# Optimization experiments

Measured on AMD Instinct MI355X. Metric: run time of the kernel, lower is better.

The kernel has to match this reference:

```python
import jax, jax.numpy as jnp
import numpy as np

TEMPERATURE = 0.2

def setup_inputs() -> dict:
    key = jax.random.key(0)
    k1, k2 = jax.random.split(key)
    B, D = 4096, 128
    emb_i = jax.random.normal(k1, (B, D), dtype=jnp.float32)
    emb_j = jax.random.normal(k2, (B, D), dtype=jnp.float32)
    return {"emb_i": emb_i, "emb_j": emb_j}

def reference(emb_i, emb_j):
    # L2-normalize each embedding row, concat -> z: [2B, D]
    z_i = emb_i / jnp.linalg.norm(emb_i, axis=1, keepdims=True)
    z_j = emb_j / jnp.linalg.norm(emb_j, axis=1, keepdims=True)
    z = jnp.concatenate([z_i, z_j], axis=0)          # [2B, D]
    N2 = z.shape[0]
    N = N2 // 2
    # cosine similarity of normalized vectors == dot product
    sim = z @ z.T                                    # [2B, 2B]
    logits = sim / TEMPERATURE
    # denominator excludes only the diagonal (k != i)
    diag_mask = jnp.eye(N2, dtype=bool)
    masked = jnp.where(diag_mask, -jnp.inf, logits)
    lse = jax.nn.logsumexp(masked, axis=1)           # [2B]
    # positive pair for row i is i+N (mod 2N)
    pos_idx = jnp.concatenate([jnp.arange(N) + N, jnp.arange(N)])
    pos_logits = jnp.take_along_axis(logits, pos_idx[:, None], axis=1)[:, 0]
    # loss = (1/2N) * sum_i -log( exp(pos_i) / sum_{k!=i} exp(logits[i,k]) )
    loss = jnp.mean(lse - pos_logits)
    return loss
```

## Files before the change

kernel.cpp:

```cpp
#include <hip/hip_runtime.h>
#include <hip/hip_bf16.h>

typedef __attribute__((ext_vector_type(8))) short bf16x8;
typedef __attribute__((ext_vector_type(4))) float f32x4;

#define EXP_SCALE 7.213475204444817f

__device__ __forceinline__ float fast_exp2(float x) {
#if __has_builtin(__builtin_amdgcn_exp2f)
  return __builtin_amdgcn_exp2f(x);
#else
  return exp2f(x);
#endif
}

__device__ __forceinline__ unsigned short f32_to_bf16(float f) {
  unsigned int u = __float_as_uint(f);
  unsigned int r = (u + 0x7FFFu + ((u >> 16) & 1u)) >> 16;
  return (unsigned short)r;
}


__global__ __launch_bounds__(256) void k_normalize(
    const float* __restrict__ emb_i, const float* __restrict__ emb_j,
    unsigned short* __restrict__ z, float* __restrict__ out)
{
  if (blockIdx.x == 0 && threadIdx.x == 0) out[0] = 0.0f;
  const int t = threadIdx.x;
  const int c = t >> 4;
  const int sub = t & 15;
  const int row = (blockIdx.x << 4) + c;
  const float* src = (row < 4096) ? (emb_i + row * 128) : (emb_j + (row - 4096) * 128);
  float4 v0 = reinterpret_cast<const float4*>(src)[sub * 2];
  float4 v1 = reinterpret_cast<const float4*>(src)[sub * 2 + 1];
  float ss = v0.x*v0.x + v0.y*v0.y + v0.z*v0.z + v0.w*v0.w
           + v1.x*v1.x + v1.y*v1.y + v1.z*v1.z + v1.w*v1.w;
  #pragma unroll
  for (int m = 1; m < 16; m <<= 1) ss += __shfl_xor(ss, m, 64);
  float rinv = 1.0f / sqrtf(ss);
  unsigned short st[8];
  st[0] = f32_to_bf16(v0.x * rinv); st[1] = f32_to_bf16(v0.y * rinv);
  st[2] = f32_to_bf16(v0.z * rinv); st[3] = f32_to_bf16(v0.w * rinv);
  st[4] = f32_to_bf16(v1.x * rinv); st[5] = f32_to_bf16(v1.y * rinv);
  st[6] = f32_to_bf16(v1.z * rinv); st[7] = f32_to_bf16(v1.w * rinv);
  unsigned short* dst = z + blockIdx.x * 2048 + (sub >> 2) * 512 +
                        (((sub & 3) << 4) + c) * 8;
  *reinterpret_cast<bf16x8*>(dst) = *reinterpret_cast<bf16x8*>(st);
}

__global__ __launch_bounds__(256, 3) void k_simlse(
    const unsigned short* __restrict__ z,
    float* __restrict__ rpart,
    float* __restrict__ cpart,
    float* __restrict__ rowpos)
{
  const int w = threadIdx.x >> 6;
  const int lane = threadIdx.x & 63;
  const int q = lane >> 4;
  const int c = lane & 15;

  int ch = 0;
  while ((int)blockIdx.x >= 4 * (ch + 1) * (ch + 2)) ++ch;
  const int rb = blockIdx.x - 4 * ch * (ch + 1);
  const int R0 = rb << 6;
  const bool upper = (rb < (ch << 3));

  bf16x8 a[4][4];
  {
    const unsigned short* ap = z + (R0 >> 4) * 2048 + (lane << 3);
    #pragma unroll
    for (int rg = 0; rg < 4; ++rg)
      #pragma unroll
      for (int kk = 0; kk < 4; ++kk)
        a[rg][kk] = *reinterpret_cast<const bf16x8*>(ap + rg * 2048 + kk * 512);
  }

  float acc[4][4];
  #pragma unroll
  for (int rg = 0; rg < 4; ++rg)
    #pragma unroll
    for (int e = 0; e < 4; ++e) acc[rg][e] = 0.0f;
  float pacc[4] = {0.f, 0.f, 0.f, 0.f};
  float colp[8];
  #pragma unroll
  for (int i = 0; i < 8; ++i) colp[i] = 0.0f;

  __shared__ float lsum[4][64];
  __shared__ float lpos[4][16];

  const int ct0 = (ch << 5) + w;
  const unsigned short* bwave = z + ct0 * 2048 + (lane << 3);

  const int pos0t = ((R0 + 4096) & 8191) >> 4;
  const int ipb = ((pos0t >> 5) == ch) ? ((pos0t & 31) >> 2) : -99;

  bf16x8 b0[4], b1[4];
  auto ldb = [&](bf16x8 (&dst)[4], int idx) {
    const unsigned short* p = bwave + idx * 8192;
    dst[0] = *reinterpret_cast<const bf16x8*>(p);
    dst[1] = *reinterpret_cast<const bf16x8*>(p + 512);
    dst[2] = *reinterpret_cast<const bf16x8*>(p + 1024);
    dst[3] = *reinterpret_cast<const bf16x8*>(p + 1536);
  };

  auto process = [&](const bf16x8 (&bb)[4], int i) {
    f32x4 cc[4];
    #pragma unroll
    for (int rr = 0; rr < 4; ++rr) cc[rr] = f32x4{0.f, 0.f, 0.f, 0.f};
    #pragma unroll
    for (int kk = 0; kk < 4; ++kk)
      #pragma unroll
      for (int rr = 0; rr < 4; ++rr)
        cc[rr] = __builtin_amdgcn_mfma_f32_16x16x32_bf16(
            a[rr][kk], bb[kk], cc[rr], 0, 0, 0);
    float cp0 = 0.0f, cp1 = 0.0f;
    #pragma unroll
    for (int rr = 0; rr < 4; ++rr)
      #pragma unroll
      for (int e = 0; e < 4; ++e) {
        float tv = fast_exp2(__builtin_fmaf(cc[rr][e], EXP_SCALE, -EXP_SCALE));
        acc[rr][e] += tv;
        if (upper) { if (rr & 1) cp1 += tv; else cp0 += tv; }
      }
    if (upper) colp[i] = cp0 + cp1;
    if (i == ipb) {
      #pragma unroll
      for (int rr = 0; rr < 4; ++rr) {
        if (rr == w) {
          #pragma unroll
          for (int e = 0; e < 4; ++e)
            if (c == ((q << 2) + e)) pacc[e] = cc[rr][e] * 5.0f;
        }
      }
    }
  };

  ldb(b0, 0);
  #pragma unroll 1
  for (int i = 0; i < 8; i += 2) {
    ldb(b1, i + 1);
    process(b0, i);
    if (i + 2 < 8) ldb(b0, i + 2);
    process(b1, i + 1);
  }

  if (upper) {
    #pragma unroll
    for (int i = 0; i < 8; ++i) {
      float v = colp[i];
      v += __shfl_xor(v, 16, 64);
      v += __shfl_xor(v, 32, 64);
      if (lane < 16)
        cpart[(rb << 13) + (((ct0 + (i << 2)) << 4) + c)] = v;
    }
  }

  #pragma unroll
  for (int m = 1; m < 16; m <<= 1) {
    #pragma unroll
    for (int rg = 0; rg < 4; ++rg)
      #pragma unroll
      for (int e = 0; e < 4; ++e)
        acc[rg][e] += __shfl_xor(acc[rg][e], m, 64);
    #pragma unroll
    for (int e = 0; e < 4; ++e) pacc[e] += __shfl_xor(pacc[e], m, 64);
  }

  if (c == 0) {
    #pragma unroll
    for (int rg = 0; rg < 4; ++rg)
      #pragma unroll
      for (int e = 0; e < 4; ++e)
        lsum[w][rg * 16 + (q << 2) + e] = acc[rg][e];
    #pragma unroll
    for (int e = 0; e < 4; ++e) lpos[w][(q << 2) + e] = pacc[e];
  }
  __syncthreads();

  if (threadIdx.x < 64) {
    const int t = threadIdx.x;
    float s = lsum[0][t] + lsum[1][t] + lsum[2][t] + lsum[3][t];
    rpart[(ch << 13) + R0 + t] = s;
    if (ipb != -99)
      rowpos[R0 + t] = lpos[t >> 4][t & 15];
  }
}

__global__ __launch_bounds__(256) void k_finish(
    const float* __restrict__ rpart, const float* __restrict__ cpart,
    const float* __restrict__ rowpos, float* __restrict__ out)
{
  const int r = blockIdx.x * 256 + threadIdx.x;
  const int chr = r >> 9;
  float t0 = -1.0f, t1 = 0.0f;
  for (int ch = chr; ch < 16; ++ch) t0 += rpart[(ch << 13) + r];
  const int nrb = chr << 3;
  #pragma unroll 4
  for (int rb = 0; rb < nrb; rb += 2) {
    t0 += cpart[(rb << 13) + r];
    t1 += cpart[((rb + 1) << 13) + r];
  }
  float tot = t0 + t1;
  float v = 5.0f + logf(tot) - rowpos[r & 4095];
  #pragma unroll
  for (int m = 1; m < 64; m <<= 1) v += __shfl_xor(v, m, 64);
  __shared__ float red[4];
  if ((threadIdx.x & 63) == 0) red[threadIdx.x >> 6] = v;
  __syncthreads();
  if (threadIdx.x == 0)
    atomicAdd(out, (red[0] + red[1] + red[2] + red[3]) * (1.0f / 8192.0f));
}

extern "C" void kernel_launch(void* const* d_in, const int* in_sizes, int n_in,
                              void* d_out, int out_size, void* d_ws, size_t ws_size,
                              hipStream_t stream) {
  const float* emb_i = (const float*)d_in[0];
  const float* emb_j = (const float*)d_in[1];
  unsigned short* z = (unsigned short*)d_ws;
  float* rpart = (float*)((char*)d_ws + (2 << 20));
  float* cpart = rpart + 16 * 8192;
  float* rowpos = cpart + 128 * 8192;
  float* out = (float*)d_out;

  k_normalize<<<512, 256, 0, stream>>>(emb_i, emb_j, z, out);
  k_simlse<<<1088, 256, 0, stream>>>(z, rpart, cpart, rowpos);
  k_finish<<<32, 256, 0, stream>>>(rpart, cpart, rowpos, out);
}
```

Before: 82.91 us.

## Switch similarity GEMM to FP8 MFMA and reduce row sums with atomics

Normalized embeddings are now quantized to FP8 e4m3 instead of bf16, and the similarity tiles use the fp8 16x16x32 MFMA with 8-byte operand loads, halving the bytes moved per tile. The per-chunk row and column partial buffers are replaced by float atomicAdds into a single rowsum array, zeroed in the normalize kernel, which shrinks the finish kernel to one read per row. Occupancy hint is raised from 3 to 4 blocks per CU. FP8 quantization loses precision in logits scaled by 1/temperature, which risks exceeding the accuracy tolerance, and atomics make the summation order nondeterministic.

```diff
diff --git a/kernel.cpp b/kernel.cpp
--- a/kernel.cpp
+++ b/kernel.cpp
@@ -1,8 +1,9 @@
 #include <hip/hip_runtime.h>
 #include <hip/hip_bf16.h>
-
-typedef __attribute__((ext_vector_type(8))) short bf16x8;
+#include <hip/hip_fp8.h>
+
 typedef __attribute__((ext_vector_type(4))) float f32x4;
+typedef long long i64;
 
 #define EXP_SCALE 7.213475204444817f
 
@@ -14,18 +15,14 @@
 #endif
 }
 
-__device__ __forceinline__ unsigned short f32_to_bf16(float f) {
-  unsigned int u = __float_as_uint(f);
-  unsigned int r = (u + 0x7FFFu + ((u >> 16) & 1u)) >> 16;
-  return (unsigned short)r;
-}
-
 
 __global__ __launch_bounds__(256) void k_normalize(
     const float* __restrict__ emb_i, const float* __restrict__ emb_j,
-    unsigned short* __restrict__ z, float* __restrict__ out)
+    unsigned char* __restrict__ z, float* __restrict__ rowsum,
+    float* __restrict__ out)
 {
   if (blockIdx.x == 0 && threadIdx.x == 0) out[0] = 0.0f;
+  if (threadIdx.x < 16) rowsum[(blockIdx.x << 4) + threadIdx.x] = 0.0f;
   const int t = threadIdx.x;
   const int c = t >> 4;
   const int sub = t & 15;
@@ -38,20 +35,23 @@
   #pragma unroll
   for (int m = 1; m < 16; m <<= 1) ss += __shfl_xor(ss, m, 64);
   float rinv = 1.0f / sqrtf(ss);
-  unsigned short st[8];
-  st[0] = f32_to_bf16(v0.x * rinv); st[1] = f32_to_bf16(v0.y * rinv);
-  st[2] = f32_to_bf16(v0.z * rinv); st[3] = f32_to_bf16(v0.w * rinv);
-  st[4] = f32_to_bf16(v1.x * rinv); st[5] = f32_to_bf16(v1.y * rinv);
-  st[6] = f32_to_bf16(v1.z * rinv); st[7] = f32_to_bf16(v1.w * rinv);
-  unsigned short* dst = z + blockIdx.x * 2048 + (sub >> 2) * 512 +
-                        (((sub & 3) << 4) + c) * 8;
-  *reinterpret_cast<bf16x8*>(dst) = *reinterpret_cast<bf16x8*>(st);
-}
-
-__global__ __launch_bounds__(256, 3) void k_simlse(
-    const unsigned short* __restrict__ z,
-    float* __restrict__ rpart,
-    float* __restrict__ cpart,
+  unsigned char st[8];
+  st[0] = __hip_fp8_e4m3(v0.x * rinv).__x;
+  st[1] = __hip_fp8_e4m3(v0.y * rinv).__x;
+  st[2] = __hip_fp8_e4m3(v0.z * rinv).__x;
+  st[3] = __hip_fp8_e4m3(v0.w * rinv).__x;
+  st[4] = __hip_fp8_e4m3(v1.x * rinv).__x;
+  st[5] = __hip_fp8_e4m3(v1.y * rinv).__x;
+  st[6] = __hip_fp8_e4m3(v1.z * rinv).__x;
+  st[7] = __hip_fp8_e4m3(v1.w * rinv).__x;
+  unsigned char* dst = z + blockIdx.x * 2048 + (sub >> 2) * 512 +
+                       (((sub & 3) << 4) + c) * 8;
+  *reinterpret_cast<i64*>(dst) = *reinterpret_cast<i64*>(st);
+}
+
+__global__ __launch_bounds__(256, 4) void k_simlse(
+    const unsigned char* __restrict__ z,
+    float* __restrict__ rowsum,
     float* __restrict__ rowpos)
 {
   const int w = threadIdx.x >> 6;
@@ -65,14 +65,14 @@
   const int R0 = rb << 6;
   const bool upper = (rb < (ch << 3));
 
-  bf16x8 a[4][4];
+  i64 a[4][4];
   {
-    const unsigned short* ap = z + (R0 >> 4) * 2048 + (lane << 3);
+    const unsigned char* ap = z + (R0 >> 4) * 2048 + (lane << 3);
     #pragma unroll
     for (int rg = 0; rg < 4; ++rg)
       #pragma unroll
       for (int kk = 0; kk < 4; ++kk)
-        a[rg][kk] = *reinterpret_cast<const bf16x8*>(ap + rg * 2048 + kk * 512);
+        a[rg][kk] = *reinterpret_cast<const i64*>(ap + rg * 2048 + kk * 512);
   }
 
   float acc[4][4];
@@ -89,21 +89,21 @@
   __shared__ float lpos[4][16];
 
   const int ct0 = (ch << 5) + w;
-  const unsigned short* bwave = z + ct0 * 2048 + (lane << 3);
+  const unsigned char* bwave = z + ct0 * 2048 + (lane << 3);
 
   const int pos0t = ((R0 + 4096) & 8191) >> 4;
   const int ipb = ((pos0t >> 5) == ch) ? ((pos0t & 31) >> 2) : -99;
 
-  bf16x8 b0[4], b1[4];
-  auto ldb = [&](bf16x8 (&dst)[4], int idx) {
-    const unsigned short* p = bwave + idx * 8192;
-    dst[0] = *reinterpret_cast<const bf16x8*>(p);
-    dst[1] = *reinterpret_cast<const bf16x8*>(p + 512);
-    dst[2] = *reinterpret_cast<const bf16x8*>(p + 1024);
-    dst[3] = *reinterpret_cast<const bf16x8*>(p + 1536);
+  i64 b0[4], b1[4];
+  auto ldb = [&](i64 (&dst)[4], int idx) {
+    const unsigned char* p = bwave + idx * 8192;
+    dst[0] = *reinterpret_cast<const i64*>(p);
+    dst[1] = *reinterpret_cast<const i64*>(p + 512);
+    dst[2] = *reinterpret_cast<const i64*>(p + 1024);
+    dst[3] = *reinterpret_cast<const i64*>(p + 1536);
   };
 
-  auto process = [&](const bf16x8 (&bb)[4], int i) {
+  auto process = [&](const i64 (&bb)[4], int i) {
     f32x4 cc[4];
     #pragma unroll
     for (int rr = 0; rr < 4; ++rr) cc[rr] = f32x4{0.f, 0.f, 0.f, 0.f};
@@ -111,7 +111,7 @@
     for (int kk = 0; kk < 4; ++kk)
       #pragma unroll
       for (int rr = 0; rr < 4; ++rr)
-        cc[rr] = __builtin_amdgcn_mfma_f32_16x16x32_bf16(
+        cc[rr] = __builtin_amdgcn_mfma_f32_16x16x32_fp8_fp8(
             a[rr][kk], bb[kk], cc[rr], 0, 0, 0);
     float cp0 = 0.0f, cp1 = 0.0f;
     #pragma unroll
@@ -151,7 +151,7 @@
       v += __shfl_xor(v, 16, 64);
       v += __shfl_xor(v, 32, 64);
       if (lane < 16)
-        cpart[(rb << 13) + (((ct0 + (i << 2)) << 4) + c)] = v;
+        atomicAdd(&rowsum[((ct0 + (i << 2)) << 4) + c], v);
     }
   }
 
@@ -180,27 +180,18 @@
   if (threadIdx.x < 64) {
     const int t = threadIdx.x;
     float s = lsum[0][t] + lsum[1][t] + lsum[2][t] + lsum[3][t];
-    rpart[(ch << 13) + R0 + t] = s;
+    atomicAdd(&rowsum[R0 + t], s);
     if (ipb != -99)
       rowpos[R0 + t] = lpos[t >> 4][t & 15];
   }
 }
 
 __global__ __launch_bounds__(256) void k_finish(
-    const float* __restrict__ rpart, const float* __restrict__ cpart,
-    const float* __restrict__ rowpos, float* __restrict__ out)
+    const float* __restrict__ rowsum, const float* __restrict__ rowpos,
+    float* __restrict__ out)
 {
   const int r = blockIdx.x * 256 + threadIdx.x;
-  const int chr = r >> 9;
-  float t0 = -1.0f, t1 = 0.0f;
-  for (int ch = chr; ch < 16; ++ch) t0 += rpart[(ch << 13) + r];
-  const int nrb = chr << 3;
-  #pragma unroll 4
-  for (int rb = 0; rb < nrb; rb += 2) {
-    t0 += cpart[(rb << 13) + r];
-    t1 += cpart[((rb + 1) << 13) + r];
-  }
-  float tot = t0 + t1;
+  float tot = rowsum[r] - 1.0f;
   float v = 5.0f + logf(tot) - rowpos[r & 4095];
   #pragma unroll
   for (int m = 1; m < 64; m <<= 1) v += __shfl_xor(v, m, 64);
@@ -216,13 +207,12 @@
                               hipStream_t stream) {
   const float* emb_i = (const float*)d_in[0];
   const float* emb_j = (const float*)d_in[1];
-  unsigned short* z = (unsigned short*)d_ws;
-  float* rpart = (float*)((char*)d_ws + (2 << 20));
-  float* cpart = rpart + 16 * 8192;
-  float* rowpos = cpart + 128 * 8192;
+  unsigned char* z = (unsigned char*)d_ws;
+  float* rowsum = (float*)((char*)d_ws + (1 << 20));
+  float* rowpos = rowsum + 8192;
   float* out = (float*)d_out;
 
-  k_normalize<<<512, 256, 0, stream>>>(emb_i, emb_j, z, out);
-  k_simlse<<<1088, 256, 0, stream>>>(z, rpart, cpart, rowpos);
-  k_finish<<<32, 256, 0, stream>>>(rpart, cpart, rowpos, out);
-}
+  k_normalize<<<512, 256, 0, stream>>>(emb_i, emb_j, z, rowsum, out);
+  k_simlse<<<1088, 256, 0, stream>>>(z, rowsum, rowpos);
+  k_finish<<<32, 256, 0, stream>>>(rowsum, rowpos, out);
+}
```

New measurement: 76.14 us, median of 2. 8.2% less time.
